# Kernel tuning notes

Measured on AMD Instinct MI355X. Metric: run time of the kernel, lower is better.

## Reference

```python
import jax, jax.numpy as jnp
import numpy as np

B, S, D, H, WIN = 2, 2048, 1024, 16, 128
DH = D // H


def setup_inputs() -> dict:
    key = jax.random.key(0)
    ks = jax.random.split(key, 6)
    sc = D ** -0.5
    return {
        "x": jax.random.normal(ks[0], (B, S, D), jnp.float32),
        "in_proj_w": jax.random.normal(ks[1], (3 * D, D), jnp.float32) * sc,
        "in_proj_b": jnp.zeros((3 * D,), jnp.float32),
        "out_proj_w": jax.random.normal(ks[2], (D, D), jnp.float32) * sc,
        "out_proj_b": jnp.zeros((D,), jnp.float32),
        "ln1_g": jnp.ones((D,), jnp.float32),
        "ln1_b": jnp.zeros((D,), jnp.float32),
        "spec_wr": jax.random.normal(ks[3], (S // 2 + 1, D), jnp.float32) * 0.02 + 1.0,
        "spec_wi": jax.random.normal(ks[4], (S // 2 + 1, D), jnp.float32) * 0.02,
        "ln2_g": jnp.ones((D,), jnp.float32),
        "ln2_b": jnp.zeros((D,), jnp.float32),
    }


def _layernorm(x, g, b, eps=1e-5):
    mu = jnp.mean(x, axis=-1, keepdims=True)
    var = jnp.mean(jnp.square(x - mu), axis=-1, keepdims=True)
    return (x - mu) * jax.lax.rsqrt(var + eps) * g + b


def reference(x, in_proj_w, in_proj_b, out_proj_w, out_proj_b,
              ln1_g, ln1_b, spec_wr, spec_wi, ln2_g, ln2_b):
    b, s, d = x.shape
    # --- sliding-window MHA (torch nn.MultiheadAttention math) ---
    qkv = x @ in_proj_w.T + in_proj_b            # [B,S,3D]
    q, k, v = jnp.split(qkv, 3, axis=-1)
    q = q.reshape(b, s, H, DH)
    k = k.reshape(b, s, H, DH)
    v = v.reshape(b, s, H, DH)
    scores = jnp.einsum('bqhd,bkhd->bhqk', q, k) * (DH ** -0.5)
    idx = jnp.arange(s)
    band_mask = jnp.abs(idx[:, None] - idx[None, :]) > WIN  # True = masked
    scores = jnp.where(band_mask[None, None], -jnp.inf, scores)
    probs = jax.nn.softmax(scores, axis=-1)
    attn = jnp.einsum('bhqk,bkhd->bqhd', probs, v).reshape(b, s, d)
    attn_out = attn @ out_proj_w.T + out_proj_b
    x_attn = _layernorm(x + attn_out, ln1_g, ln1_b)
    # --- spectral block: rfft along seq, learned complex filter, irfft ---
    Xf = jnp.fft.rfft(x, axis=1)                  # [B, S//2+1, D] complex
    Wc = spec_wr + 1j * spec_wi
    x_wave = jnp.fft.irfft(Xf * Wc[None], n=s, axis=1).astype(x.dtype)
    # --- mix ---
    return _layernorm(x_attn + x_wave, ln2_g, ln2_b)
```

## Files before the change

kernel.cpp:

```cpp
#include <hip/hip_runtime.h>
#include <hip/hip_bf16.h>
#include <math.h>

#define BB    2
#define SS    2048
#define DD    1024
#define HH    16
#define DHH   64
#define WINW  128
#define MROWS (BB * SS)

typedef __attribute__((ext_vector_type(8))) short short8;
typedef __attribute__((ext_vector_type(4))) short short4v;
typedef __attribute__((ext_vector_type(4))) float floatx4;

__device__ __forceinline__ float bf2f(short s) {
  union { unsigned u; float f; } t;
  t.u = ((unsigned)(unsigned short)s) << 16;
  return t.f;
}

__device__ inline void load16_lds(const __hip_bfloat16* g, __hip_bfloat16* l) {
  __builtin_amdgcn_global_load_lds(
      (const __attribute__((address_space(1))) uint32_t*)g,
      (__attribute__((address_space(3))) uint32_t*)l, 16, 0, 0);
}

__global__ __launch_bounds__(256) void prep_fused(
    const float* __restrict__ x, __hip_bfloat16* __restrict__ xT_bf,
    __hip_bfloat16* __restrict__ x_bf,
    const float* __restrict__ w_in, const float* __restrict__ w_out,
    __hip_bfloat16* __restrict__ w_in_bf, __hip_bfloat16* __restrict__ w_out_bf,
    const float* __restrict__ wr, const float* __restrict__ wi,
    __hip_bfloat16* __restrict__ wrT, __hip_bfloat16* __restrict__ wiT) {
  __shared__ float tile[64][65];
  const int id = blockIdx.x;
  const int tx = threadIdx.x & 63;
  const int ty = threadIdx.x >> 6;

  if (id < 1024) {
    const int bz = id >> 9;
    const int rem = id & 511;
    const int c0 = (rem & 15) * 64;
    const int r0 = (rem >> 4) * 64;
    const size_t base = (size_t)bz * SS * DD;
#pragma unroll
    for (int i = 0; i < 16; ++i) {
      const int r = ty * 16 + i;
      const float v = x[base + (size_t)(r0 + r) * DD + c0 + tx];
      tile[r][tx] = v;
      x_bf[base + (size_t)(r0 + r) * DD + c0 + tx] = __float2bfloat16(v);
    }
    __syncthreads();
#pragma unroll
    for (int i = 0; i < 16; ++i) {
      const int c = ty * 16 + i;
      xT_bf[base + (size_t)(c0 + c) * SS + r0 + tx] = __float2bfloat16(tile[tx][c]);
    }
  } else if (id < 2048) {
    const int blk = id - 1024;
    const float* src; __hip_bfloat16* dst; size_t off;
    if (blk < 768) { src = w_in; dst = w_in_bf; off = (size_t)blk * 4096; }
    else { src = w_out; dst = w_out_bf; off = (size_t)(blk - 768) * 4096; }
#pragma unroll
    for (int c = 0; c < 4; ++c) {
      const size_t j = off + c * 1024 + threadIdx.x * 4;
      const float4 v = *(const float4*)(src + j);
      dst[j + 0] = __float2bfloat16(v.x);
      dst[j + 1] = __float2bfloat16(v.y);
      dst[j + 2] = __float2bfloat16(v.z);
      dst[j + 3] = __float2bfloat16(v.w);
    }
  } else {
    const int id2 = id - 2048;
    const int half = id2 >= 272;
    const int rem = id2 - (half ? 272 : 0);
    const float* src = half ? wi : wr;
    __hip_bfloat16* dst = half ? wiT : wrT;
    const int R = 1025, C = DD;
    const int c0 = (rem & 15) * 64;
    const int r0 = (rem >> 4) * 64;
#pragma unroll
    for (int i = 0; i < 16; ++i) {
      const int r = ty * 16 + i;
      if (r0 + r < R) tile[r][tx] = src[(size_t)(r0 + r) * C + c0 + tx];
    }
    __syncthreads();
#pragma unroll
    for (int i = 0; i < 16; ++i) {
      const int c = ty * 16 + i;
      if (r0 + tx < R) dst[(size_t)(c0 + c) * R + r0 + tx] = __float2bfloat16(tile[tx][c]);
    }
  }
}

template <bool BF16OUT>
__device__ __forceinline__ void gemm_tile128(
    const __hip_bfloat16* __restrict__ A, const __hip_bfloat16* __restrict__ B,
    const float* __restrict__ bias, void* __restrict__ Cp,
    int N, int K, int row0, int col0, __hip_bfloat16* sm) {
  __hip_bfloat16* As0 = sm;
  __hip_bfloat16* As1 = sm + 4096;
  __hip_bfloat16* Bs0 = sm + 8192;
  __hip_bfloat16* Bs1 = sm + 12288;
  const int tid  = threadIdx.x;
  const int lane = tid & 63;
  const int wave = tid >> 6;
  const int wrow = (wave >> 1) * 64;
  const int wcol = (wave & 1) * 64;
  const int srow = tid >> 2;
  const int skk  = (tid & 3) * 8;
  const int quad = lane >> 4;
  const int l16  = lane & 15;
  floatx4 acc[4][4] = {};
  for (int k0 = 0; k0 < K; k0 += 64) {
    __syncthreads();
    load16_lds(A + (size_t)(row0 + srow) * K + k0 + skk,           &As0[tid * 8]);
    load16_lds(A + (size_t)(row0 + 64 + srow) * K + k0 + skk,      &As0[2048 + tid * 8]);
    load16_lds(A + (size_t)(row0 + srow) * K + k0 + 32 + skk,      &As1[tid * 8]);
    load16_lds(A + (size_t)(row0 + 64 + srow) * K + k0 + 32 + skk, &As1[2048 + tid * 8]);
    load16_lds(B + (size_t)(col0 + srow) * K + k0 + skk,           &Bs0[tid * 8]);
    load16_lds(B + (size_t)(col0 + 64 + srow) * K + k0 + skk,      &Bs0[2048 + tid * 8]);
    load16_lds(B + (size_t)(col0 + srow) * K + k0 + 32 + skk,      &Bs1[tid * 8]);
    load16_lds(B + (size_t)(col0 + 64 + srow) * K + k0 + 32 + skk, &Bs1[2048 + tid * 8]);
    __syncthreads();
    {
      short8 af[4], bf[4];
#pragma unroll
      for (int i = 0; i < 4; ++i)
        af[i] = *(const short8*)&As0[(wrow + i * 16 + l16) * 32 + quad * 8];
#pragma unroll
      for (int j = 0; j < 4; ++j)
        bf[j] = *(const short8*)&Bs0[(wcol + j * 16 + l16) * 32 + quad * 8];
#pragma unroll
      for (int i = 0; i < 4; ++i)
#pragma unroll
        for (int j = 0; j < 4; ++j)
          acc[i][j] = __builtin_amdgcn_mfma_f32_16x16x32_bf16(af[i], bf[j], acc[i][j], 0, 0, 0);
    }
    {
      short8 af[4], bf[4];
#pragma unroll
      for (int i = 0; i < 4; ++i)
        af[i] = *(const short8*)&As1[(wrow + i * 16 + l16) * 32 + quad * 8];
#pragma unroll
      for (int j = 0; j < 4; ++j)
        bf[j] = *(const short8*)&Bs1[(wcol + j * 16 + l16) * 32 + quad * 8];
#pragma unroll
      for (int i = 0; i < 4; ++i)
#pragma unroll
        for (int j = 0; j < 4; ++j)
          acc[i][j] = __builtin_amdgcn_mfma_f32_16x16x32_bf16(af[i], bf[j], acc[i][j], 0, 0, 0);
    }
  }
#pragma unroll
  for (int i = 0; i < 4; ++i) {
#pragma unroll
    for (int j = 0; j < 4; ++j) {
      const int col = col0 + wcol + j * 16 + l16;
      const float bs = bias[col];
#pragma unroll
      for (int r = 0; r < 4; ++r) {
        const int row = row0 + wrow + i * 16 + quad * 4 + r;
        if (BF16OUT)
          ((__hip_bfloat16*)Cp)[(size_t)row * N + col] = __float2bfloat16(acc[i][j][r] + bs);
        else
          ((float*)Cp)[(size_t)row * N + col] = acc[i][j][r] + bs;
      }
    }
  }
}

#define PAD2(a) ((a) + ((a) >> 5))

__device__ __forceinline__ void spec_body(
    int sid, __hip_bfloat16* __restrict__ xw,
    const __hip_bfloat16* __restrict__ wrT, const __hip_bfloat16* __restrict__ wiT,
    float* smf) {
  float2* cx = (float2*)smf;
  const int tid = threadIdx.x;
  const int dpair = sid & 511;
  const int b = sid >> 9;
  const int d0 = dpair * 2, d1 = d0 + 1;
  __hip_bfloat16* col0 = xw + ((size_t)b * DD + d0) * SS;
  __hip_bfloat16* col1 = xw + ((size_t)b * DD + d1) * SS;

  for (int s4 = tid * 4; s4 < SS; s4 += 1024) {
    const short4v a = *(const short4v*)(col0 + s4);
    const short4v c = *(const short4v*)(col1 + s4);
    const int p = PAD2(s4);
    cx[p + 0] = float2{bf2f(a[0]), bf2f(c[0])};
    cx[p + 1] = float2{bf2f(a[1]), bf2f(c[1])};
    cx[p + 2] = float2{bf2f(a[2]), bf2f(c[2])};
    cx[p + 3] = float2{bf2f(a[3]), bf2f(c[3])};
  }

#pragma unroll
  for (int s = 11; s >= 3; s -= 2) {
    __syncthreads();
    const int h2 = 1 << (s - 2);
    const float ang = -6.283185307179586f / (float)(1 << s);
#pragma unroll 2
    for (int g = tid; g < 512; g += 256) {
      const int q = g & (h2 - 1);
      const int base = ((g >> (s - 2)) << s) + q;
      const int i0 = PAD2(base), i1 = PAD2(base + h2);
      const int i2 = PAD2(base + 2 * h2), i3 = PAD2(base + 3 * h2);
      float sn, cn;
      __sincosf(ang * (float)q, &sn, &cn);
      const float2 A = cx[i0], B = cx[i1], C = cx[i2], D = cx[i3];
      const float2 Ap = {A.x + C.x, A.y + C.y};
      const float acx = A.x - C.x, acy = A.y - C.y;
      const float2 Cp = {acx * cn - acy * sn, acx * sn + acy * cn};
      const float2 Bp = {B.x + D.x, B.y + D.y};
      const float bdx = B.x - D.x, bdy = B.y - D.y;
      const float2 Dp = {bdx * sn + bdy * cn, bdy * sn - bdx * cn};
      const float w3r = cn * cn - sn * sn, w3i = 2.f * cn * sn;
      cx[i0] = float2{Ap.x + Bp.x, Ap.y + Bp.y};
      const float abx = Ap.x - Bp.x, aby = Ap.y - Bp.y;
      cx[i1] = float2{abx * w3r - aby * w3i, abx * w3i + aby * w3r};
      cx[i2] = float2{Cp.x + Dp.x, Cp.y + Dp.y};
      const float cdx = Cp.x - Dp.x, cdy = Cp.y - Dp.y;
      cx[i3] = float2{cdx * w3r - cdy * w3i, cdx * w3i + cdy * w3r};
    }
  }
  __syncthreads();
  for (int t = tid; t < 1024; t += 256) {
    const int i = PAD2(2 * t), j = PAD2(2 * t + 1);
    const float2 a = cx[i], b = cx[j];
    cx[i] = float2{a.x + b.x, a.y + b.y};
    cx[j] = float2{a.x - b.x, a.y - b.y};
  }
  __syncthreads();

  const __hip_bfloat16* w0r = wrT + (size_t)d0 * 1025;
  const __hip_bfloat16* w0i = wiT + (size_t)d0 * 1025;
  const __hip_bfloat16* w1r = wrT + (size_t)d1 * 1025;
  const __hip_bfloat16* w1i = wiT + (size_t)d1 * 1025;
  const float sc = 1.0f / (float)SS;
  for (int k = tid; k < 1024; k += 256) {
    if (k == 0) {
      const float2 z0 = cx[0];
      cx[0] = float2{z0.x * __bfloat162float(w0r[0]) * sc,
                     z0.y * __bfloat162float(w1r[0]) * sc};
      const float2 zn = cx[1];
      cx[1] = float2{zn.x * __bfloat162float(w0r[1024]) * sc,
                     zn.y * __bfloat162float(w1r[1024]) * sc};
    } else {
      const int p1 = PAD2(__brev((unsigned)k) >> 21);
      const int p2 = PAD2(__brev((unsigned)(SS - k)) >> 21);
      const float2 A = cx[p1];
      const float2 Bv = cx[p2];
      const float z0r = 0.5f * (A.x + Bv.x), z0i = 0.5f * (A.y - Bv.y);
      const float z1r = 0.5f * (A.y + Bv.y), z1i = -0.5f * (A.x - Bv.x);
      const float a0 = __bfloat162float(w0r[k]) * sc, b0 = __bfloat162float(w0i[k]) * sc;
      const float a1 = __bfloat162float(w1r[k]) * sc, b1 = __bfloat162float(w1i[k]) * sc;
      const float y0r = z0r * a0 - z0i * b0, y0i = z0r * b0 + z0i * a0;
      const float y1r = z1r * a1 - z1i * b1, y1i = z1r * b1 + z1i * a1;
      cx[p1] = float2{y0r - y1i, y0i + y1r};
      cx[p2] = float2{y0r + y1i, y1r - y0i};
    }
  }

#pragma unroll
  for (int s = 1; s <= 9; s += 2) {
    __syncthreads();
    const int h = 1 << (s - 1);
    const float ang = -6.283185307179586f / (float)(1 << (s + 1));
#pragma unroll 2
    for (int g = tid; g < 512; g += 256) {
      const int q = g & (h - 1);
      const int base = ((g >> (s - 1)) << (s + 1)) + q;
      const int i0 = PAD2(base), i1 = PAD2(base + h);
      const int i2 = PAD2(base + 2 * h), i3 = PAD2(base + 3 * h);
      float sn, cn;
      __sincosf(ang * (float)q, &sn, &cn);
      const float wpr = cn, wpi = -sn;
      const float wsr = cn * cn - sn * sn, wsi = -2.f * cn * sn;
      const float2 A = cx[i0], B = cx[i1], C = cx[i2], D = cx[i3];
      const float2 tB = {B.x * wsr - B.y * wsi, B.x * wsi + B.y * wsr};
      const float2 tD = {D.x * wsr - D.y * wsi, D.x * wsi + D.y * wsr};
      const float2 Ap = {A.x + tB.x, A.y + tB.y};
      const float2 Bp = {A.x - tB.x, A.y - tB.y};
      const float2 Cp = {C.x + tD.x, C.y + tD.y};
      const float2 Dp = {C.x - tD.x, C.y - tD.y};
      const float2 u = {Cp.x * wpr - Cp.y * wpi, Cp.x * wpi + Cp.y * wpr};
      const float2 v = {Dp.x * sn - Dp.y * cn, Dp.x * cn + Dp.y * sn};
      cx[i0] = float2{Ap.x + u.x, Ap.y + u.y};
      cx[i2] = float2{Ap.x - u.x, Ap.y - u.y};
      cx[i1] = float2{Bp.x + v.x, Bp.y + v.y};
      cx[i3] = float2{Bp.x - v.x, Bp.y - v.y};
    }
  }
  __syncthreads();
  for (int p = tid; p < 1024; p += 256) {
    float sn, cn;
    __sincosf(-6.283185307179586f * (float)p * (1.0f / 2048.0f), &sn, &cn);
    const int i = PAD2(p), j = PAD2(p + 1024);
    const float2 a = cx[i], b = cx[j];
    const float tr = b.x * cn + b.y * sn;
    const float ti = b.y * cn - b.x * sn;
    cx[i] = float2{a.x + tr, a.y + ti};
    cx[j] = float2{a.x - tr, a.y - ti};
  }
  __syncthreads();

  for (int s4 = tid * 4; s4 < SS; s4 += 1024) {
    const int p = PAD2(s4);
    const float2 v0 = cx[p + 0], v1 = cx[p + 1], v2 = cx[p + 2], v3 = cx[p + 3];
    short4v a, c;
    a[0] = (short)__bfloat16_as_ushort(__float2bfloat16(v0.x));
    a[1] = (short)__bfloat16_as_ushort(__float2bfloat16(v1.x));
    a[2] = (short)__bfloat16_as_ushort(__float2bfloat16(v2.x));
    a[3] = (short)__bfloat16_as_ushort(__float2bfloat16(v3.x));
    c[0] = (short)__bfloat16_as_ushort(__float2bfloat16(v0.y));
    c[1] = (short)__bfloat16_as_ushort(__float2bfloat16(v1.y));
    c[2] = (short)__bfloat16_as_ushort(__float2bfloat16(v2.y));
    c[3] = (short)__bfloat16_as_ushort(__float2bfloat16(v3.y));
    *(short4v*)(col0 + s4) = a;
    *(short4v*)(col1 + s4) = c;
  }
}

__global__ __launch_bounds__(256) void gemm1_spec(
    const __hip_bfloat16* __restrict__ x_bf, const __hip_bfloat16* __restrict__ w_in_bf,
    const float* __restrict__ in_b, __hip_bfloat16* __restrict__ qkv_bf,
    __hip_bfloat16* __restrict__ xT_bf, const __hip_bfloat16* __restrict__ wrT,
    const __hip_bfloat16* __restrict__ wiT) {
  extern __shared__ __align__(16) char smem[];
  if (blockIdx.x < 768) {
    const int id = blockIdx.x;
    const int col0 = (id % 24) * 128;
    const int row0 = (id / 24) * 128;
    gemm_tile128<true>(x_bf, w_in_bf, in_b, qkv_bf, 3 * DD, DD, row0, col0,
                       (__hip_bfloat16*)smem);
  } else {
    spec_body(blockIdx.x - 768, xT_bf, wrT, wiT, (float*)smem);
  }
}

__global__ __launch_bounds__(256) void gemm2_tback(
    const __hip_bfloat16* __restrict__ attn_bf, const __hip_bfloat16* __restrict__ w_out_bf,
    const float* __restrict__ out_b, __hip_bfloat16* __restrict__ attn_out_bf,
    const __hip_bfloat16* __restrict__ xT_bf, __hip_bfloat16* __restrict__ x_wave_bf) {
  extern __shared__ __align__(16) char smem[];
  if (blockIdx.x < 256) {
    const int id = blockIdx.x;
    const int col0 = (id % 8) * 128;
    const int row0 = (id / 8) * 128;
    gemm_tile128<true>(attn_bf, w_out_bf, out_b, attn_out_bf, DD, DD, row0, col0,
                       (__hip_bfloat16*)smem);
  } else {
    float (*tile)[65] = (float(*)[65])smem;
    const int id = blockIdx.x - 256;
    const int bz = id >> 9;
    const int rem = id & 511;
    const int s0 = (rem >> 4) * 64;
    const int d0 = (rem & 15) * 64;
    const int tx = threadIdx.x & 63;
    const int ty = threadIdx.x >> 6;
    const __hip_bfloat16* src = xT_bf + (size_t)bz * DD * SS;
    __hip_bfloat16* dst = x_wave_bf + (size_t)bz * SS * DD;
#pragma unroll
    for (int i = 0; i < 16; ++i) {
      const int r = ty * 16 + i;
      tile[r][tx] = __bfloat162float(src[(size_t)(d0 + r) * SS + s0 + tx]);
    }
    __syncthreads();
#pragma unroll
    for (int i = 0; i < 16; ++i) {
      const int c = ty * 16 + i;
      dst[(size_t)(s0 + c) * DD + d0 + tx] = __float2bfloat16(tile[tx][c]);
    }
  }
}

__global__ __launch_bounds__(256, 2) void attn_mfma(
    const __hip_bfloat16* __restrict__ qkv, __hip_bfloat16* __restrict__ attn) {
  __shared__ __attribute__((aligned(16))) __hip_bfloat16 QsA[64 * 32];
  __shared__ __attribute__((aligned(16))) __hip_bfloat16 QsB[64 * 32];
  __shared__ __attribute__((aligned(16))) __hip_bfloat16 KsA[160 * 32];
  __shared__ __attribute__((aligned(16))) __hip_bfloat16 KsB[160 * 32];
  __shared__ __attribute__((aligned(16))) __hip_bfloat16 Vt[64 * 168];
  __shared__ __attribute__((aligned(16))) __hip_bfloat16 Ps[64 * 168];

  const int tid  = threadIdx.x;
  const int lane = tid & 63;
  const int w    = tid >> 6;
  const int quad = lane >> 4;
  const int l16  = lane & 15;
  const int q0   = blockIdx.x * 64;
  const int h    = blockIdx.y;
  const int b    = blockIdx.z;
  const int kbase = q0 - WINW;

  const int r_ = tid >> 2;
  const int c8 = (tid & 3) * 8;

  {
    const __hip_bfloat16* src = qkv + ((size_t)(b * SS + q0 + r_)) * (3 * DD) + h * DHH;
    load16_lds(src + c8,      &QsA[r_ * 32 + c8]);
    load16_lds(src + 32 + c8, &QsB[r_ * 32 + c8]);
  }

  short8 qf0, qf1;
  float m_run[4] = {-1e30f, -1e30f, -1e30f, -1e30f};
  float l_run[4] = {0.f, 0.f, 0.f, 0.f};
  floatx4 ob[4] = {};

  for (int c = 0; c < 2; ++c) {
    const int ck0 = kbase + c * 160;
    __syncthreads();
#pragma unroll
    for (int it = 0; it < 3; ++it) {
      const int r = it * 64 + r_;
      if (r < 160) {
        int key = ck0 + r; key = key < 0 ? 0 : (key > SS - 1 ? SS - 1 : key);
        const __hip_bfloat16* src = qkv + ((size_t)(b * SS + key)) * (3 * DD) + DD + h * DHH;
        load16_lds(src + c8,      &KsA[r * 32 + c8]);
        load16_lds(src + 32 + c8, &KsB[r * 32 + c8]);
      }
    }
    {
      const int k4 = (tid >> 3) * 4;
      const int d8 = (tid & 7) * 8;
#pragma unroll
      for (int it = 0; it < 2; ++it) {
        const int rr = it * 128 + k4;
        if (rr < 160) {
          short8 v[4];
#pragma unroll
          for (int u = 0; u < 4; ++u) {
            int key = ck0 + rr + u; key = key < 0 ? 0 : (key > SS - 1 ? SS - 1 : key);
            v[u] = *(const short8*)(qkv + ((size_t)(b * SS + key)) * (3 * DD) + 2 * DD + h * DHH + d8);
          }
#pragma unroll
          for (int j = 0; j < 8; ++j) {
            short4v pk; pk[0] = v[0][j]; pk[1] = v[1][j]; pk[2] = v[2][j]; pk[3] = v[3][j];
            *(short4v*)&Vt[(d8 + j) * 168 + rr] = pk;
          }
        }
      }
    }
    __syncthreads();

    if (c == 0) {
      qf0 = *(const short8*)&QsA[(w * 16 + l16) * 32 + quad * 8];
      qf1 = *(const short8*)&QsB[(w * 16 + l16) * 32 + quad * 8];
    }

    floatx4 sc[10];
#pragma unroll
    for (int kt = 0; kt < 10; ++kt) {
      const short8 bk0 = *(const short8*)&KsA[(kt * 16 + l16) * 32 + quad * 8];
      const short8 bk1 = *(const short8*)&KsB[(kt * 16 + l16) * 32 + quad * 8];
      floatx4 a = {};
      a = __builtin_amdgcn_mfma_f32_16x16x32_bf16(qf0, bk0, a, 0, 0, 0);
      a = __builtin_amdgcn_mfma_f32_16x16x32_bf16(qf1, bk1, a, 0, 0, 0);
      sc[kt] = a;
    }

    float cm[4] = {-1e30f, -1e30f, -1e30f, -1e30f};
#pragma unroll
    for (int kt = 0; kt < 10; ++kt) {
      const int key = ck0 + kt * 16 + l16;
#pragma unroll
      for (int r = 0; r < 4; ++r) {
        const int qq = q0 + w * 16 + quad * 4 + r;
        const int dqk = qq - key;
        const bool ok = (key >= 0) & (key < SS) & (dqk <= WINW) & (dqk >= -WINW);
        const float s = ok ? sc[kt][r] * 0.125f : -1e30f;
        sc[kt][r] = s;
        cm[r] = fmaxf(cm[r], s);
      }
    }
#pragma unroll
    for (int off = 1; off < 16; off <<= 1)
#pragma unroll
      for (int r = 0; r < 4; ++r) cm[r] = fmaxf(cm[r], __shfl_xor(cm[r], off, 64));

    float alpha[4], csum[4] = {0.f, 0.f, 0.f, 0.f};
#pragma unroll
    for (int r = 0; r < 4; ++r) {
      const float mn = fmaxf(m_run[r], cm[r]);
      alpha[r] = __expf(m_run[r] - mn);
      m_run[r] = mn;
    }

    __hip_bfloat16* Pw = &Ps[w * 16 * 168];
#pragma unroll
    for (int kt = 0; kt < 10; ++kt) {
#pragma unroll
      for (int r = 0; r < 4; ++r) {
        const float p = __expf(sc[kt][r] - m_run[r]);
        csum[r] += p;
        Pw[(quad * 4 + r) * 168 + kt * 16 + l16] = __float2bfloat16(p);
      }
    }
#pragma unroll
    for (int off = 1; off < 16; off <<= 1)
#pragma unroll
      for (int r = 0; r < 4; ++r) csum[r] += __shfl_xor(csum[r], off, 64);
#pragma unroll
    for (int r = 0; r < 4; ++r) l_run[r] = l_run[r] * alpha[r] + csum[r];
#pragma unroll
    for (int t = 0; t < 4; ++t)
#pragma unroll
      for (int r = 0; r < 4; ++r) ob[t][r] *= alpha[r];

#pragma unroll
    for (int kt = 0; kt < 5; ++kt) {
      const short8 pf = *(const short8*)&Pw[l16 * 168 + kt * 32 + quad * 8];
#pragma unroll
      for (int t = 0; t < 4; ++t) {
        const short8 vf = *(const short8*)&Vt[(t * 16 + l16) * 168 + kt * 32 + quad * 8];
        ob[t] = __builtin_amdgcn_mfma_f32_16x16x32_bf16(pf, vf, ob[t], 0, 0, 0);
      }
    }
  }

  float inv[4];
#pragma unroll
  for (int r = 0; r < 4; ++r) inv[r] = 1.f / l_run[r];
  const int qq0 = q0 + w * 16 + quad * 4;
#pragma unroll
  for (int t = 0; t < 4; ++t)
#pragma unroll
    for (int r = 0; r < 4; ++r)
      attn[((size_t)(b * SS + qq0 + r)) * DD + h * DHH + t * 16 + l16] =
          __float2bfloat16(ob[t][r] * inv[r]);
}

__global__ __launch_bounds__(256) void ln_fused(
    const float* __restrict__ x, const __hip_bfloat16* __restrict__ attn_out,
    const float* __restrict__ g1, const float* __restrict__ b1,
    const __hip_bfloat16* __restrict__ xwave,
    const float* __restrict__ g2, const float* __restrict__ b2,
    float* __restrict__ out) {
  const int row = blockIdx.x;
  const int tid = threadIdx.x;
  const int lane = tid & 63;
  const int wave = tid >> 6;
  __shared__ float red[8];

  const float4 xv = *(const float4*)(x + (size_t)row * DD + tid * 4);
  const short4v av = *(const short4v*)(attn_out + (size_t)row * DD + tid * 4);
  float v[4] = {xv.x + bf2f(av[0]), xv.y + bf2f(av[1]),
                xv.z + bf2f(av[2]), xv.w + bf2f(av[3])};

  float s = v[0] + v[1] + v[2] + v[3];
  float s2 = v[0] * v[0] + v[1] * v[1] + v[2] * v[2] + v[3] * v[3];
#pragma unroll
  for (int off = 32; off; off >>= 1) {
    s += __shfl_xor(s, off, 64);
    s2 += __shfl_xor(s2, off, 64);
  }
  if (lane == 0) { red[wave] = s; red[4 + wave] = s2; }
  __syncthreads();
  s = red[0] + red[1] + red[2] + red[3];
  s2 = red[4] + red[5] + red[6] + red[7];
  float mu = s * (1.f / DD);
  float var = s2 * (1.f / DD) - mu * mu;
  float r = rsqrtf(var + 1e-5f);

  const float4 g1v = *(const float4*)(g1 + tid * 4);
  const float4 b1v = *(const float4*)(b1 + tid * 4);
  const short4v wv = *(const short4v*)(xwave + (size_t)row * DD + tid * 4);
  float a[4];
  a[0] = (v[0] - mu) * r * g1v.x + b1v.x + bf2f(wv[0]);
  a[1] = (v[1] - mu) * r * g1v.y + b1v.y + bf2f(wv[1]);
  a[2] = (v[2] - mu) * r * g1v.z + b1v.z + bf2f(wv[2]);
  a[3] = (v[3] - mu) * r * g1v.w + b1v.w + bf2f(wv[3]);

  s = a[0] + a[1] + a[2] + a[3];
  s2 = a[0] * a[0] + a[1] * a[1] + a[2] * a[2] + a[3] * a[3];
#pragma unroll
  for (int off = 32; off; off >>= 1) {
    s += __shfl_xor(s, off, 64);
    s2 += __shfl_xor(s2, off, 64);
  }
  __syncthreads();
  if (lane == 0) { red[wave] = s; red[4 + wave] = s2; }
  __syncthreads();
  s = red[0] + red[1] + red[2] + red[3];
  s2 = red[4] + red[5] + red[6] + red[7];
  mu = s * (1.f / DD);
  var = s2 * (1.f / DD) - mu * mu;
  r = rsqrtf(var + 1e-5f);

  const float4 g2v = *(const float4*)(g2 + tid * 4);
  const float4 b2v = *(const float4*)(b2 + tid * 4);
  float4 o;
  o.x = (a[0] - mu) * r * g2v.x + b2v.x;
  o.y = (a[1] - mu) * r * g2v.y + b2v.y;
  o.z = (a[2] - mu) * r * g2v.z + b2v.z;
  o.w = (a[3] - mu) * r * g2v.w + b2v.w;
  *(float4*)(out + (size_t)row * DD + tid * 4) = o;
}

extern "C" void kernel_launch(void* const* d_in, const int* in_sizes, int n_in,
                              void* d_out, int out_size, void* d_ws, size_t ws_size,
                              hipStream_t stream) {
  const float* x     = (const float*)d_in[0];
  const float* in_w  = (const float*)d_in[1];
  const float* in_b  = (const float*)d_in[2];
  const float* out_w = (const float*)d_in[3];
  const float* out_b = (const float*)d_in[4];
  const float* ln1_g = (const float*)d_in[5];
  const float* ln1_b = (const float*)d_in[6];
  const float* wr    = (const float*)d_in[7];
  const float* wi    = (const float*)d_in[8];
  const float* ln2_g = (const float*)d_in[9];
  const float* ln2_b = (const float*)d_in[10];
  float* out = (float*)d_out;

  char* ws = (char*)d_ws;
  __hip_bfloat16* xT_bf    = (__hip_bfloat16*)(ws);
  __hip_bfloat16* x_bf     = (__hip_bfloat16*)(ws + 16777216);
  __hip_bfloat16* attn_bf  = (__hip_bfloat16*)(ws + 16777216);
  __hip_bfloat16* w_in_bf  = (__hip_bfloat16*)(ws + 25165824);
  __hip_bfloat16* w_out_bf = (__hip_bfloat16*)(ws + 31457280);
  __hip_bfloat16* qkv_bf   = (__hip_bfloat16*)(ws + 33554432);
  __hip_bfloat16* attn_out_bf = (__hip_bfloat16*)(ws + 33554432);
  __hip_bfloat16* x_wave_bf   = (__hip_bfloat16*)(ws + 44040192);
  __hip_bfloat16* wrT      = (__hip_bfloat16*)(ws + 58720256);
  __hip_bfloat16* wiT      = (__hip_bfloat16*)(ws + 60819456);

  prep_fused<<<2592, 256, 0, stream>>>(x, xT_bf, x_bf, in_w, out_w,
                                       w_in_bf, w_out_bf, wr, wi, wrT, wiT);

  gemm1_spec<<<1792, 256, 32768, stream>>>(x_bf, w_in_bf, in_b, qkv_bf,
                                           xT_bf, wrT, wiT);

  attn_mfma<<<dim3(SS / 64, HH, BB), 256, 0, stream>>>(qkv_bf, attn_bf);

  gemm2_tback<<<1280, 256, 32768, stream>>>(attn_bf, w_out_bf, out_b,
                                            attn_out_bf, xT_bf, x_wave_bf);

  ln_fused<<<MROWS, 256, 0, stream>>>(x, attn_out_bf, ln1_g, ln1_b,
                                      x_wave_bf, ln2_g, ln2_b, out);
}
```

Before: 215.6 us.

## Split-K the output projection and sum the partials in the fused layernorm

The output-projection GEMM is split into two K-halves, giving 512 tiles instead of 256 so the GPU is better filled. Each half writes a bf16 partial without bias, and the fused layernorm kernel adds both partials plus the bias. The layernorm also reads the bf16 copy of x instead of the fp32 input to save bandwidth, which costs some residual precision. The workspace layout is changed so x_bf and both partial buffers stay alive until the layernorm runs.

```diff
diff --git a/kernel.cpp b/kernel.cpp
--- a/kernel.cpp
+++ b/kernel.cpp
@@ -94,11 +94,10 @@
   }
 }
 
-template <bool BF16OUT>
 __device__ __forceinline__ void gemm_tile128(
     const __hip_bfloat16* __restrict__ A, const __hip_bfloat16* __restrict__ B,
-    const float* __restrict__ bias, void* __restrict__ Cp,
-    int N, int K, int row0, int col0, __hip_bfloat16* sm) {
+    const float* __restrict__ bias, __hip_bfloat16* __restrict__ Cp,
+    int N, int Kloop, int ld, int row0, int col0, __hip_bfloat16* sm) {
   __hip_bfloat16* As0 = sm;
   __hip_bfloat16* As1 = sm + 4096;
   __hip_bfloat16* Bs0 = sm + 8192;
@@ -113,16 +112,16 @@
   const int quad = lane >> 4;
   const int l16  = lane & 15;
   floatx4 acc[4][4] = {};
-  for (int k0 = 0; k0 < K; k0 += 64) {
-    __syncthreads();
-    load16_lds(A + (size_t)(row0 + srow) * K + k0 + skk,           &As0[tid * 8]);
-    load16_lds(A + (size_t)(row0 + 64 + srow) * K + k0 + skk,      &As0[2048 + tid * 8]);
-    load16_lds(A + (size_t)(row0 + srow) * K + k0 + 32 + skk,      &As1[tid * 8]);
-    load16_lds(A + (size_t)(row0 + 64 + srow) * K + k0 + 32 + skk, &As1[2048 + tid * 8]);
-    load16_lds(B + (size_t)(col0 + srow) * K + k0 + skk,           &Bs0[tid * 8]);
-    load16_lds(B + (size_t)(col0 + 64 + srow) * K + k0 + skk,      &Bs0[2048 + tid * 8]);
-    load16_lds(B + (size_t)(col0 + srow) * K + k0 + 32 + skk,      &Bs1[tid * 8]);
-    load16_lds(B + (size_t)(col0 + 64 + srow) * K + k0 + 32 + skk, &Bs1[2048 + tid * 8]);
+  for (int k0 = 0; k0 < Kloop; k0 += 64) {
+    __syncthreads();
+    load16_lds(A + (size_t)(row0 + srow) * ld + k0 + skk,           &As0[tid * 8]);
+    load16_lds(A + (size_t)(row0 + 64 + srow) * ld + k0 + skk,      &As0[2048 + tid * 8]);
+    load16_lds(A + (size_t)(row0 + srow) * ld + k0 + 32 + skk,      &As1[tid * 8]);
+    load16_lds(A + (size_t)(row0 + 64 + srow) * ld + k0 + 32 + skk, &As1[2048 + tid * 8]);
+    load16_lds(B + (size_t)(col0 + srow) * ld + k0 + skk,           &Bs0[tid * 8]);
+    load16_lds(B + (size_t)(col0 + 64 + srow) * ld + k0 + skk,      &Bs0[2048 + tid * 8]);
+    load16_lds(B + (size_t)(col0 + srow) * ld + k0 + 32 + skk,      &Bs1[tid * 8]);
+    load16_lds(B + (size_t)(col0 + 64 + srow) * ld + k0 + 32 + skk, &Bs1[2048 + tid * 8]);
     __syncthreads();
     {
       short8 af[4], bf[4];
@@ -158,14 +157,11 @@
 #pragma unroll
     for (int j = 0; j < 4; ++j) {
       const int col = col0 + wcol + j * 16 + l16;
-      const float bs = bias[col];
+      const float bs = bias ? bias[col] : 0.f;
 #pragma unroll
       for (int r = 0; r < 4; ++r) {
         const int row = row0 + wrow + i * 16 + quad * 4 + r;
-        if (BF16OUT)
-          ((__hip_bfloat16*)Cp)[(size_t)row * N + col] = __float2bfloat16(acc[i][j][r] + bs);
-        else
-          ((float*)Cp)[(size_t)row * N + col] = acc[i][j][r] + bs;
+        Cp[(size_t)row * N + col] = __float2bfloat16(acc[i][j][r] + bs);
       }
     }
   }
@@ -332,8 +328,8 @@
     const int id = blockIdx.x;
     const int col0 = (id % 24) * 128;
     const int row0 = (id / 24) * 128;
-    gemm_tile128<true>(x_bf, w_in_bf, in_b, qkv_bf, 3 * DD, DD, row0, col0,
-                       (__hip_bfloat16*)smem);
+    gemm_tile128(x_bf, w_in_bf, in_b, qkv_bf, 3 * DD, DD, DD, row0, col0,
+                 (__hip_bfloat16*)smem);
   } else {
     spec_body(blockIdx.x - 768, xT_bf, wrT, wiT, (float*)smem);
   }
@@ -341,18 +337,20 @@
 
 __global__ __launch_bounds__(256) void gemm2_tback(
     const __hip_bfloat16* __restrict__ attn_bf, const __hip_bfloat16* __restrict__ w_out_bf,
-    const float* __restrict__ out_b, __hip_bfloat16* __restrict__ attn_out_bf,
+    __hip_bfloat16* __restrict__ p0, __hip_bfloat16* __restrict__ p1,
     const __hip_bfloat16* __restrict__ xT_bf, __hip_bfloat16* __restrict__ x_wave_bf) {
   extern __shared__ __align__(16) char smem[];
-  if (blockIdx.x < 256) {
-    const int id = blockIdx.x;
-    const int col0 = (id % 8) * 128;
-    const int row0 = (id / 8) * 128;
-    gemm_tile128<true>(attn_bf, w_out_bf, out_b, attn_out_bf, DD, DD, row0, col0,
-                       (__hip_bfloat16*)smem);
+  if (blockIdx.x < 512) {
+    const int t = blockIdx.x & 255;
+    const int kh = blockIdx.x >> 8;
+    const int col0 = (t % 8) * 128;
+    const int row0 = (t / 8) * 128;
+    gemm_tile128(attn_bf + kh * 512, w_out_bf + kh * 512, nullptr,
+                 kh ? p1 : p0, DD, 512, DD, row0, col0,
+                 (__hip_bfloat16*)smem);
   } else {
     float (*tile)[65] = (float(*)[65])smem;
-    const int id = blockIdx.x - 256;
+    const int id = blockIdx.x - 512;
     const int bz = id >> 9;
     const int rem = id & 511;
     const int s0 = (rem >> 4) * 64;
@@ -532,7 +530,9 @@
 }
 
 __global__ __launch_bounds__(256) void ln_fused(
-    const float* __restrict__ x, const __hip_bfloat16* __restrict__ attn_out,
+    const __hip_bfloat16* __restrict__ x_bf,
+    const __hip_bfloat16* __restrict__ p0, const __hip_bfloat16* __restrict__ p1,
+    const float* __restrict__ out_b,
     const float* __restrict__ g1, const float* __restrict__ b1,
     const __hip_bfloat16* __restrict__ xwave,
     const float* __restrict__ g2, const float* __restrict__ b2,
@@ -543,10 +543,15 @@
   const int wave = tid >> 6;
   __shared__ float red[8];
 
-  const float4 xv = *(const float4*)(x + (size_t)row * DD + tid * 4);
-  const short4v av = *(const short4v*)(attn_out + (size_t)row * DD + tid * 4);
-  float v[4] = {xv.x + bf2f(av[0]), xv.y + bf2f(av[1]),
-                xv.z + bf2f(av[2]), xv.w + bf2f(av[3])};
+  const short4v xv = *(const short4v*)(x_bf + (size_t)row * DD + tid * 4);
+  const short4v a0 = *(const short4v*)(p0 + (size_t)row * DD + tid * 4);
+  const short4v a1 = *(const short4v*)(p1 + (size_t)row * DD + tid * 4);
+  const float4 obv = *(const float4*)(out_b + tid * 4);
+  float v[4];
+  v[0] = bf2f(xv[0]) + bf2f(a0[0]) + bf2f(a1[0]) + obv.x;
+  v[1] = bf2f(xv[1]) + bf2f(a0[1]) + bf2f(a1[1]) + obv.y;
+  v[2] = bf2f(xv[2]) + bf2f(a0[2]) + bf2f(a1[2]) + obv.z;
+  v[3] = bf2f(xv[3]) + bf2f(a0[3]) + bf2f(a1[3]) + obv.w;
 
   float s = v[0] + v[1] + v[2] + v[3];
   float s2 = v[0] * v[0] + v[1] * v[1] + v[2] * v[2] + v[3] * v[3];
@@ -616,13 +621,14 @@
 
   char* ws = (char*)d_ws;
   __hip_bfloat16* xT_bf    = (__hip_bfloat16*)(ws);
-  __hip_bfloat16* x_bf     = (__hip_bfloat16*)(ws + 16777216);
+  __hip_bfloat16* x_bf     = (__hip_bfloat16*)(ws + 8388608);
   __hip_bfloat16* attn_bf  = (__hip_bfloat16*)(ws + 16777216);
   __hip_bfloat16* w_in_bf  = (__hip_bfloat16*)(ws + 25165824);
   __hip_bfloat16* w_out_bf = (__hip_bfloat16*)(ws + 31457280);
   __hip_bfloat16* qkv_bf   = (__hip_bfloat16*)(ws + 33554432);
-  __hip_bfloat16* attn_out_bf = (__hip_bfloat16*)(ws + 33554432);
-  __hip_bfloat16* x_wave_bf   = (__hip_bfloat16*)(ws + 44040192);
+  __hip_bfloat16* p0       = (__hip_bfloat16*)(ws + 33554432);
+  __hip_bfloat16* p1       = (__hip_bfloat16*)(ws + 41943040);
+  __hip_bfloat16* x_wave_bf= (__hip_bfloat16*)(ws + 50331648);
   __hip_bfloat16* wrT      = (__hip_bfloat16*)(ws + 58720256);
   __hip_bfloat16* wiT      = (__hip_bfloat16*)(ws + 60819456);
 
@@ -634,9 +640,9 @@
 
   attn_mfma<<<dim3(SS / 64, HH, BB), 256, 0, stream>>>(qkv_bf, attn_bf);
 
-  gemm2_tback<<<1280, 256, 32768, stream>>>(attn_bf, w_out_bf, out_b,
-                                            attn_out_bf, xT_bf, x_wave_bf);
-
-  ln_fused<<<MROWS, 256, 0, stream>>>(x, attn_out_bf, ln1_g, ln1_b,
+  gemm2_tback<<<1536, 256, 32768, stream>>>(attn_bf, w_out_bf, p0, p1,
+                                            xT_bf, x_wave_bf);
+
+  ln_fused<<<MROWS, 256, 0, stream>>>(x_bf, p0, p1, out_b, ln1_g, ln1_b,
                                       x_wave_bf, ln2_g, ln2_b, out);
 }
```

Result: faster. 210.6 us, median of 3 (-2.3%).
